# Optimization experiments

Hardware: AMD Instinct MI355X
Metric: run time of the kernel (lower is better)

Reference implementation:

```python
import jax, jax.numpy as jnp
import numpy as np
from jax import lax

EPS = 1e-7  # keras.backend.epsilon()
DT = 0.05

def _k(a):
    # (3,3) -> HWIO (3,3,1,1) fp32 kernel constant
    return jnp.asarray(np.asarray(a, dtype=np.float32).reshape(3, 3, 1, 1))

KXP = _k([[0,0,0],[0,-1,1],[0,0,0]])
KXN = _k([[0,0,0],[-1,1,0],[0,0,0]])
KYP = _k([[0,1,0],[0,-1,0],[0,0,0]])
KYN = _k([[0,0,0],[0,1,0],[0,-1,0]])
KXC = _k([[0,0,0],[-1,0,1],[0,0,0]])
KYC = _k([[0,1,0],[0,0,0],[0,-1,0]])
KLX = _k([[1,0,-1],[2,0,-2],[1,0,-1]])
KLY = _k([[1,2,1],[0,0,0],[-1,-2,-1]])

def conv(x, k):
    # TF K.conv2d 'same' == XLA cross-correlation, NHWC/HWIO
    return lax.conv_general_dilated(x, k, (1, 1), 'SAME',
                                    dimension_numbers=('NHWC', 'HWIO', 'NHWC'))

def setup_inputs() -> dict:
    key = jax.random.key(0)
    k1, k2 = jax.random.split(key)
    B, H, W = 32, 512, 512
    u = jax.random.normal(k1, (B, H, W, 1), dtype=jnp.float32)
    img = jax.random.uniform(k2, (B, H, W, 1), dtype=jnp.float32)
    alpha = jnp.ones((1, 1, 1, 1), jnp.float32)
    beta = jnp.ones((1, 1, 1, 1), jnp.float32)
    gamma = jnp.ones((1, 1, 1, 1), jnp.float32)
    return {"u": u, "img": img, "alpha": alpha, "beta": beta, "gamma": gamma}

def reference(u, img, alpha, beta, gamma):
    # --- edge stopping function g(img) (precomputed in build() in original) ---
    ex = conv(img, KLX)
    ey = conv(img, KLY)
    edges = jnp.square(jnp.square(ex) + jnp.square(ey))
    edges = edges / jnp.max(edges)
    edges = 1.0 / (edges + 1.0)
    gex = conv(edges, KXC)
    gey = conv(edges, KYC)
    # --- upwind transport term ---
    xp = conv(u, KXP); xn = conv(u, KXN)
    yp = conv(u, KYP); yn = conv(u, KYN)
    fxp = jax.nn.relu(gex); fxn = -jax.nn.relu(-gex)
    fyp = jax.nn.relu(gey); fyn = -jax.nn.relu(-gey)
    transport = 20.0 * ((fxp * xp + fxn * xn) + (fyp * yp + fyn * yn))
    # --- curvature (divergence of normalized gradient) ---
    gux = conv(u, KXC)
    guy = conv(u, KYC)
    normu = jnp.sqrt(jnp.square(gux) + jnp.square(guy) + EPS)
    kappa = conv(gux / (normu + EPS), KXC) + conv(guy / (normu + EPS), KYC)
    curvature = edges * kappa * normu
    balloon = edges * normu
    return u + DT * (curvature * alpha + transport * beta + balloon * gamma)
```

## Files before the change

kernel.cpp:

```cpp
#include <hip/hip_runtime.h>

#define HH 512
#define WW 512
#define NB 32
#define EPSF 1e-7f
#define DTF 0.05f
#define RS1 8
#define RSF 8

__device__ __forceinline__ float bperm(int addr, float v) {
    return __int_as_float(__builtin_amdgcn_ds_bpermute(addr, __float_as_int(v)));
}

struct R10 { float v[10]; };

__device__ __forceinline__ void load_row10(const float* __restrict__ base, int row,
                                           int lane, int bpu, int bpd,
                                           bool lo, bool hi, R10& r) {
    if ((unsigned)row < (unsigned)HH) {
        const float4* p = (const float4*)(base + row * WW + 8 * lane);
        float4 a = p[0], b = p[1];
        r.v[1] = a.x; r.v[2] = a.y; r.v[3] = a.z; r.v[4] = a.w;
        r.v[5] = b.x; r.v[6] = b.y; r.v[7] = b.z; r.v[8] = b.w;
    } else {
        #pragma unroll
        for (int k = 1; k <= 8; ++k) r.v[k] = 0.f;
    }
    float l = bperm(bpu, r.v[8]);
    float h = bperm(bpd, r.v[1]);
    r.v[0] = lo ? 0.f : l;
    r.v[9] = hi ? 0.f : h;
}

__global__ __launch_bounds__(256, 2)
void max_e4_kernel(const float* __restrict__ img, float* __restrict__ partial) {
    const int wid  = blockIdx.x * 4 + (threadIdx.x >> 6);
    const int lane = threadIdx.x & 63;
    const int rs = wid & 63;
    const int b  = wid >> 6;
    const int i0 = rs * RS1;
    const float* __restrict__ IM = img + (size_t)b * (HH * WW);
    const bool lo = (lane == 0), hi = (lane == 63);
    const int bpu = ((lane + 63) & 63) << 2, bpd = ((lane + 1) & 63) << 2;

    R10 A, B, C;
    load_row10(IM, i0 - 1, lane, bpu, bpd, lo, hi, A);
    load_row10(IM, i0,     lane, bpu, bpd, lo, hi, B);
    float m = 0.f;
    #pragma unroll
    for (int i = i0; i < i0 + RS1; ++i) {
        load_row10(IM, i + 1, lane, bpu, bpd, lo, hi, C);
        #pragma unroll
        for (int k = 1; k <= 8; ++k) {
            float ex = (A.v[k-1] - A.v[k+1]) + 2.f * (B.v[k-1] - B.v[k+1]) + (C.v[k-1] - C.v[k+1]);
            float ey = (A.v[k-1] - C.v[k-1]) + 2.f * (A.v[k] - C.v[k]) + (A.v[k+1] - C.v[k+1]);
            float s2 = ex * ex + ey * ey;
            m = fmaxf(m, s2 * s2);
        }
        A = B; B = C;
    }
    for (int off = 32; off > 0; off >>= 1)
        m = fmaxf(m, __shfl_down(m, off, 64));
    if (lane == 0) partial[wid] = m;
}

__global__ __launch_bounds__(256)
void reduce_max(const float* __restrict__ partial, float* __restrict__ wsmax) {
    float v = 0.f;
    #pragma unroll
    for (int k = 0; k < 8; ++k)
        v = fmaxf(v, partial[threadIdx.x + 256 * k]);
    for (int off = 32; off > 0; off >>= 1)
        v = fmaxf(v, __shfl_down(v, off, 64));
    __shared__ float smax[4];
    const int lane = threadIdx.x & 63, w = threadIdx.x >> 6;
    if (lane == 0) smax[w] = v;
    __syncthreads();
    if (threadIdx.x == 0)
        wsmax[0] = fmaxf(fmaxf(smax[0], smax[1]), fmaxf(smax[2], smax[3]));
}

__global__ __launch_bounds__(256, 2)
void fused_ff(const float* __restrict__ u, const float* __restrict__ img,
              const float* __restrict__ pa, const float* __restrict__ pb,
              const float* __restrict__ pg, const float* __restrict__ wsmax,
              float* __restrict__ out) {
    const int wid  = blockIdx.x * 4 + (threadIdx.x >> 6);
    const int lane = threadIdx.x & 63;
    const int rs = wid & 63;
    const int b  = wid >> 6;
    const int o0 = rs * RSF;
    const size_t base = (size_t)b * (HH * WW);
    const float* __restrict__ U  = u + base;
    const float* __restrict__ IM = img + base;
    float* __restrict__ O = out + base;
    const bool lo = (lane == 0), hi = (lane == 63);
    const int bpu = ((lane + 63) & 63) << 2, bpd = ((lane + 1) & 63) << 2;

    const float M   = wsmax[0];
    const float dta = DTF * pa[0];
    const float dtb = 20.f * DTF * pb[0];
    const float dtg = DTF * pg[0];

    R10 I0 = {}, I1 = {}, R1 = {}, R2 = {}, E2 = {}, PX2 = {};
    float R0[9] = {}, E1[9] = {}, PY1[9] = {}, PY2[9] = {};

    if (o0 >= 2) {
        load_row10(IM, o0 - 2, lane, bpu, bpd, lo, hi, I0);
        load_row10(IM, o0 - 1, lane, bpu, bpd, lo, hi, I1);
        load_row10(U,  o0 - 2, lane, bpu, bpd, lo, hi, R1);
        load_row10(U,  o0 - 1, lane, bpu, bpd, lo, hi, R2);
    }

    #pragma unroll
    for (int o = o0 - 2; o < o0 + RSF; ++o) {
        R10 C, W;
        load_row10(IM, o + 2, lane, bpu, bpd, lo, hi, C);
        load_row10(U,  o + 2, lane, bpu, bpd, lo, hi, W);

        float eN[10], PXN[10], PYN[9];
        if (o >= -1 && o < HH - 1) {
            #pragma unroll
            for (int k = 1; k <= 8; ++k) {
                float ex = (I0.v[k-1] - I0.v[k+1]) + 2.f * (I1.v[k-1] - I1.v[k+1]) + (C.v[k-1] - C.v[k+1]);
                float ey = (I0.v[k-1] - C.v[k-1]) + 2.f * (I0.v[k] - C.v[k]) + (I0.v[k+1] - C.v[k+1]);
                float s2 = ex * ex + ey * ey;
                eN[k] = M * __builtin_amdgcn_rcpf(s2 * s2 + M);
                float gux = R2.v[k+1] - R2.v[k-1];
                float guy = R1.v[k] - W.v[k];
                float rn  = __builtin_amdgcn_rsqf(gux * gux + guy * guy + EPSF);
                PXN[k] = gux * rn;
                PYN[k] = guy * rn;
            }
        } else {
            #pragma unroll
            for (int k = 1; k <= 8; ++k) { eN[k] = 0.f; PXN[k] = 0.f; PYN[k] = 0.f; }
        }
        {
            float a = bperm(bpu, eN[8]),  bb = bperm(bpd, eN[1]);
            float c = bperm(bpu, PXN[8]), d  = bperm(bpd, PXN[1]);
            eN[0]  = lo ? 0.f : a;  eN[9]  = hi ? 0.f : bb;
            PXN[0] = lo ? 0.f : c;  PXN[9] = hi ? 0.f : d;
        }

        if (o >= o0) {
            float vals[8];
            #pragma unroll
            for (int k = 1; k <= 8; ++k) {
                float gex = E2.v[k+1] - E2.v[k-1];
                float gey = E1[k] - eN[k];
                float xp = R1.v[k+1] - R1.v[k], xn = R1.v[k] - R1.v[k-1];
                float yp = R0[k] - R1.v[k],     yn = R1.v[k] - R2.v[k];
                float tr = fmaxf(gex, 0.f) * xp + fminf(gex, 0.f) * xn
                         + fmaxf(gey, 0.f) * yp + fminf(gey, 0.f) * yn;
                float gxc = R1.v[k+1] - R1.v[k-1], gyc = R0[k] - R2.v[k];
                float ncv = __builtin_amdgcn_sqrtf(gxc * gxc + gyc * gyc + EPSF);
                float kap = (PX2.v[k+1] - PX2.v[k-1]) + (PY1[k] - PYN[k]);
                vals[k-1] = R1.v[k] + E2.v[k] * ncv * (kap * dta + dtg) + tr * dtb;
            }
            float4* p = (float4*)(O + o * WW + 8 * lane);
            p[0] = make_float4(vals[0], vals[1], vals[2], vals[3]);
            p[1] = make_float4(vals[4], vals[5], vals[6], vals[7]);
        }

        I0 = I1; I1 = C;
        #pragma unroll
        for (int k = 1; k <= 8; ++k) { R0[k] = R1.v[k]; E1[k] = E2.v[k]; PY1[k] = PY2[k]; PY2[k] = PYN[k]; }
        R1 = R2; R2 = W;
        E2 = *(R10*)&eN[0]; PX2 = *(R10*)&PXN[0];
    }
}

extern "C" void kernel_launch(void* const* d_in, const int* in_sizes, int n_in,
                              void* d_out, int out_size, void* d_ws, size_t ws_size,
                              hipStream_t stream) {
    const float* u   = (const float*)d_in[0];
    const float* img = (const float*)d_in[1];
    const float* pa  = (const float*)d_in[2];
    const float* pb  = (const float*)d_in[3];
    const float* pg  = (const float*)d_in[4];
    float* out = (float*)d_out;
    float* partial = (float*)d_ws;
    float* wsmax   = partial + 2048;

    max_e4_kernel<<<512, 256, 0, stream>>>(img, partial);
    reduce_max<<<1, 256, 0, stream>>>(partial, wsmax);
    fused_ff<<<512, 256, 0, stream>>>(u, img, pa, pb, pg, wsmax, out);
}
```

Before: 124.3 us.

## Split stencil into column panels, double grids, fold max reduction into fused kernel

Result: slower. 175.8 us (+41.5%).

```diff
diff --git a/kernel.cpp b/kernel.cpp
--- a/kernel.cpp
+++ b/kernel.cpp
@@ -5,8 +5,9 @@
 #define NB 32
 #define EPSF 1e-7f
 #define DTF 0.05f
-#define RS1 8
+#define RS1 4
 #define RSF 8
+#define PANW 256
 
 __device__ __forceinline__ float bperm(int addr, float v) {
     return __int_as_float(__builtin_amdgcn_ds_bpermute(addr, __float_as_int(v)));
@@ -32,12 +33,12 @@
     r.v[9] = hi ? 0.f : h;
 }
 
-__global__ __launch_bounds__(256, 2)
+__global__ __launch_bounds__(256, 4)
 void max_e4_kernel(const float* __restrict__ img, float* __restrict__ partial) {
     const int wid  = blockIdx.x * 4 + (threadIdx.x >> 6);
     const int lane = threadIdx.x & 63;
-    const int rs = wid & 63;
-    const int b  = wid >> 6;
+    const int rs = wid & 127;
+    const int b  = wid >> 7;
     const int i0 = rs * RS1;
     const float* __restrict__ IM = img + (size_t)b * (HH * WW);
     const bool lo = (lane == 0), hi = (lane == 63);
@@ -64,64 +65,94 @@
     if (lane == 0) partial[wid] = m;
 }
 
-__global__ __launch_bounds__(256)
-void reduce_max(const float* __restrict__ partial, float* __restrict__ wsmax) {
-    float v = 0.f;
-    #pragma unroll
-    for (int k = 0; k < 8; ++k)
-        v = fmaxf(v, partial[threadIdx.x + 256 * k]);
-    for (int off = 32; off > 0; off >>= 1)
-        v = fmaxf(v, __shfl_down(v, off, 64));
-    __shared__ float smax[4];
-    const int lane = threadIdx.x & 63, w = threadIdx.x >> 6;
-    if (lane == 0) smax[w] = v;
-    __syncthreads();
-    if (threadIdx.x == 0)
-        wsmax[0] = fmaxf(fmaxf(smax[0], smax[1]), fmaxf(smax[2], smax[3]));
-}
-
-__global__ __launch_bounds__(256, 2)
+struct R7 { float v[6]; float x; };
+
+__device__ __forceinline__ void load_row(const float* __restrict__ base, int row,
+                                         int lane, int c0, int bpu, int bpd,
+                                         bool actL, bool actR, bool zL, bool zR, R7& r) {
+    if ((unsigned)row < (unsigned)HH) {
+        const float* rp = base + (size_t)row * WW;
+        const float4 a = *(const float4*)(rp + c0 + 4 * lane);
+        r.v[1] = a.x; r.v[2] = a.y; r.v[3] = a.z; r.v[4] = a.w;
+        float l = bperm(bpu, r.v[4]);
+        float h = bperm(bpd, r.v[1]);
+        float xx = 0.f;
+        if (actL | actR) {
+            const float2 t = *(const float2*)(rp + (actL ? c0 - 2 : c0 + PANW));
+            if (actL) { l = t.y; xx = t.x; }
+            else      { h = t.x; xx = t.y; }
+        }
+        r.v[0] = zL ? 0.f : l;
+        r.v[5] = zR ? 0.f : h;
+        r.x = xx;
+    } else {
+        #pragma unroll
+        for (int k = 0; k < 6; ++k) r.v[k] = 0.f;
+        r.x = 0.f;
+    }
+}
+
+__global__ __launch_bounds__(256, 4)
 void fused_ff(const float* __restrict__ u, const float* __restrict__ img,
               const float* __restrict__ pa, const float* __restrict__ pb,
-              const float* __restrict__ pg, const float* __restrict__ wsmax,
+              const float* __restrict__ pg, const float* __restrict__ partial,
               float* __restrict__ out) {
+    __shared__ float sred[4];
+    {
+        float v = 0.f;
+        #pragma unroll
+        for (int k = 0; k < 16; ++k)
+            v = fmaxf(v, partial[threadIdx.x + 256 * k]);
+        for (int off = 32; off > 0; off >>= 1)
+            v = fmaxf(v, __shfl_down(v, off, 64));
+        if ((threadIdx.x & 63) == 0) sred[threadIdx.x >> 6] = v;
+    }
+    __syncthreads();
+    const float M = fmaxf(fmaxf(sred[0], sred[1]), fmaxf(sred[2], sred[3]));
+
     const int wid  = blockIdx.x * 4 + (threadIdx.x >> 6);
     const int lane = threadIdx.x & 63;
-    const int rs = wid & 63;
-    const int b  = wid >> 6;
+    const int p  = wid & 1;
+    const int rs = (wid >> 1) & 63;
+    const int b  = wid >> 7;
     const int o0 = rs * RSF;
+    const int c0 = p * PANW;
     const size_t base = (size_t)b * (HH * WW);
     const float* __restrict__ U  = u + base;
     const float* __restrict__ IM = img + base;
     float* __restrict__ O = out + base;
-    const bool lo = (lane == 0), hi = (lane == 63);
     const int bpu = ((lane + 63) & 63) << 2, bpd = ((lane + 1) & 63) << 2;
-
-    const float M   = wsmax[0];
+    const bool l0 = (lane == 0), l63 = (lane == 63);
+    const bool actL = l0  && (c0 > 0);
+    const bool actR = l63 && (c0 + PANW < WW);
+    const bool zL = l0 && !actL, zR = l63 && !actR;
+
     const float dta = DTF * pa[0];
     const float dtb = 20.f * DTF * pb[0];
     const float dtg = DTF * pg[0];
 
-    R10 I0 = {}, I1 = {}, R1 = {}, R2 = {}, E2 = {}, PX2 = {};
-    float R0[9] = {}, E1[9] = {}, PY1[9] = {}, PY2[9] = {};
+    R7 I0 = {}, I1 = {}, R1 = {}, R2 = {};
+    float E2[6] = {}, PX2[6] = {};
+    float R0[5] = {}, E1[5] = {}, PY1[5] = {}, PY2[5] = {};
 
     if (o0 >= 2) {
-        load_row10(IM, o0 - 2, lane, bpu, bpd, lo, hi, I0);
-        load_row10(IM, o0 - 1, lane, bpu, bpd, lo, hi, I1);
-        load_row10(U,  o0 - 2, lane, bpu, bpd, lo, hi, R1);
-        load_row10(U,  o0 - 1, lane, bpu, bpd, lo, hi, R2);
+        load_row(IM, o0 - 2, lane, c0, bpu, bpd, actL, actR, zL, zR, I0);
+        load_row(IM, o0 - 1, lane, c0, bpu, bpd, actL, actR, zL, zR, I1);
+        load_row(U,  o0 - 2, lane, c0, bpu, bpd, actL, actR, zL, zR, R1);
+        load_row(U,  o0 - 1, lane, c0, bpu, bpd, actL, actR, zL, zR, R2);
     }
 
     #pragma unroll
     for (int o = o0 - 2; o < o0 + RSF; ++o) {
-        R10 C, W;
-        load_row10(IM, o + 2, lane, bpu, bpd, lo, hi, C);
-        load_row10(U,  o + 2, lane, bpu, bpd, lo, hi, W);
-
-        float eN[10], PXN[10], PYN[9];
-        if (o >= -1 && o < HH - 1) {
+        R7 C, W;
+        load_row(IM, o + 2, lane, c0, bpu, bpd, actL, actR, zL, zR, C);
+        load_row(U,  o + 2, lane, c0, bpu, bpd, actL, actR, zL, zR, W);
+
+        float eN[6], PXN[6], PYN[5];
+        const bool rowv = (o >= -1) && (o < HH - 1);
+        if (rowv) {
             #pragma unroll
-            for (int k = 1; k <= 8; ++k) {
+            for (int k = 1; k <= 4; ++k) {
                 float ex = (I0.v[k-1] - I0.v[k+1]) + 2.f * (I1.v[k-1] - I1.v[k+1]) + (C.v[k-1] - C.v[k+1]);
                 float ey = (I0.v[k-1] - C.v[k-1]) + 2.f * (I0.v[k] - C.v[k]) + (I0.v[k+1] - C.v[k+1]);
                 float s2 = ex * ex + ey * ey;
@@ -134,20 +165,40 @@
             }
         } else {
             #pragma unroll
-            for (int k = 1; k <= 8; ++k) { eN[k] = 0.f; PXN[k] = 0.f; PYN[k] = 0.f; }
+            for (int k = 1; k <= 4; ++k) { eN[k] = 0.f; PXN[k] = 0.f; PYN[k] = 0.f; }
         }
         {
-            float a = bperm(bpu, eN[8]),  bb = bperm(bpd, eN[1]);
-            float c = bperm(bpu, PXN[8]), d  = bperm(bpd, PXN[1]);
-            eN[0]  = lo ? 0.f : a;  eN[9]  = hi ? 0.f : bb;
-            PXN[0] = lo ? 0.f : c;  PXN[9] = hi ? 0.f : d;
+            float a = bperm(bpu, eN[4]),  bb = bperm(bpd, eN[1]);
+            float c = bperm(bpu, PXN[4]), d  = bperm(bpd, PXN[1]);
+            eN[0]  = zL ? 0.f : a;  eN[5]  = zR ? 0.f : bb;
+            PXN[0] = zL ? 0.f : c;  PXN[5] = zR ? 0.f : d;
+        }
+        if (rowv && (actL | actR)) {
+            float i0a = actL ? I0.x    : I0.v[4];
+            float i0b = actL ? I0.v[0] : I0.v[5];
+            float i0c = actL ? I0.v[1] : I0.x;
+            float i1a = actL ? I1.x    : I1.v[4];
+            float i1c = actL ? I1.v[1] : I1.x;
+            float ca  = actL ? C.x     : C.v[4];
+            float cb  = actL ? C.v[0]  : C.v[5];
+            float cc  = actL ? C.v[1]  : C.x;
+            float ex = (i0a - i0c) + 2.f * (i1a - i1c) + (ca - cc);
+            float ey = (i0a - ca) + 2.f * (i0b - cb) + (i0c - cc);
+            float s2 = ex * ex + ey * ey;
+            float eh = M * __builtin_amdgcn_rcpf(s2 * s2 + M);
+            float gux = actL ? (R2.v[1] - R2.x)    : (R2.x - R2.v[4]);
+            float guy = actL ? (R1.v[0] - W.v[0])  : (R1.v[5] - W.v[5]);
+            float rn = __builtin_amdgcn_rsqf(gux * gux + guy * guy + EPSF);
+            float ph = gux * rn;
+            if (actL) { eN[0] = eh; PXN[0] = ph; }
+            else      { eN[5] = eh; PXN[5] = ph; }
         }
 
         if (o >= o0) {
-            float vals[8];
+            float vals[4];
             #pragma unroll
-            for (int k = 1; k <= 8; ++k) {
-                float gex = E2.v[k+1] - E2.v[k-1];
+            for (int k = 1; k <= 4; ++k) {
+                float gex = E2[k+1] - E2[k-1];
                 float gey = E1[k] - eN[k];
                 float xp = R1.v[k+1] - R1.v[k], xn = R1.v[k] - R1.v[k-1];
                 float yp = R0[k] - R1.v[k],     yn = R1.v[k] - R2.v[k];
@@ -155,19 +206,19 @@
                          + fmaxf(gey, 0.f) * yp + fminf(gey, 0.f) * yn;
                 float gxc = R1.v[k+1] - R1.v[k-1], gyc = R0[k] - R2.v[k];
                 float ncv = __builtin_amdgcn_sqrtf(gxc * gxc + gyc * gyc + EPSF);
-                float kap = (PX2.v[k+1] - PX2.v[k-1]) + (PY1[k] - PYN[k]);
-                vals[k-1] = R1.v[k] + E2.v[k] * ncv * (kap * dta + dtg) + tr * dtb;
+                float kap = (PX2[k+1] - PX2[k-1]) + (PY1[k] - PYN[k]);
+                vals[k-1] = R1.v[k] + E2[k] * ncv * (kap * dta + dtg) + tr * dtb;
             }
-            float4* p = (float4*)(O + o * WW + 8 * lane);
-            p[0] = make_float4(vals[0], vals[1], vals[2], vals[3]);
-            p[1] = make_float4(vals[4], vals[5], vals[6], vals[7]);
+            *(float4*)(O + (size_t)o * WW + c0 + 4 * lane) =
+                make_float4(vals[0], vals[1], vals[2], vals[3]);
         }
 
         I0 = I1; I1 = C;
         #pragma unroll
-        for (int k = 1; k <= 8; ++k) { R0[k] = R1.v[k]; E1[k] = E2.v[k]; PY1[k] = PY2[k]; PY2[k] = PYN[k]; }
+        for (int k = 1; k <= 4; ++k) { R0[k] = R1.v[k]; E1[k] = E2[k]; PY1[k] = PY2[k]; PY2[k] = PYN[k]; }
         R1 = R2; R2 = W;
-        E2 = *(R10*)&eN[0]; PX2 = *(R10*)&PXN[0];
+        #pragma unroll
+        for (int k = 0; k < 6; ++k) { E2[k] = eN[k]; PX2[k] = PXN[k]; }
     }
 }
 
@@ -181,9 +232,7 @@
     const float* pg  = (const float*)d_in[4];
     float* out = (float*)d_out;
     float* partial = (float*)d_ws;
-    float* wsmax   = partial + 2048;
-
-    max_e4_kernel<<<512, 256, 0, stream>>>(img, partial);
-    reduce_max<<<1, 256, 0, stream>>>(partial, wsmax);
-    fused_ff<<<512, 256, 0, stream>>>(u, img, pa, pb, pg, wsmax, out);
-}
+
+    max_e4_kernel<<<1024, 256, 0, stream>>>(img, partial);
+    fused_ff<<<1024, 256, 0, stream>>>(u, img, pa, pb, pg, partial, out);
+}
```
